# Performance work log

Hardware: AMD Instinct MI355X
Metric: run time of the kernel (lower is better)

Reference implementation:

```python
import jax, jax.numpy as jnp
import numpy as np

B, T, L = 16, 512, 128
ENC, H, E, V, A = 512, 1024, 512, 10000, 512
SOS = 1


def setup_inputs() -> dict:
    key = jax.random.key(0)
    ks = jax.random.split(key, 16)
    s = 0.02
    return {
        "enc_out": jax.random.normal(ks[0], (B, T, ENC), jnp.float32),
        "enc_lens": jax.random.randint(ks[1], (B,), T // 2, T + 1),
        "ys": jax.random.randint(ks[2], (B, L), 3, V),
        "embed": jax.random.normal(ks[3], (V, E), jnp.float32) * s,
        "W_ih0": jax.random.normal(ks[4], (4 * H, E + ENC), jnp.float32) * s,
        "W_hh0": jax.random.normal(ks[5], (4 * H, H), jnp.float32) * s,
        "b0": jnp.zeros((4 * H,), jnp.float32),
        "W_ih1": jax.random.normal(ks[6], (4 * H, H), jnp.float32) * s,
        "W_hh1": jax.random.normal(ks[7], (4 * H, H), jnp.float32) * s,
        "b1": jnp.zeros((4 * H,), jnp.float32),
        "W_enc": jax.random.normal(ks[8], (ENC, A), jnp.float32) * s,
        "b_att": jnp.zeros((A,), jnp.float32),
        "v_att": jax.random.normal(ks[9], (A,), jnp.float32) * s,
        "W_dec": jax.random.normal(ks[10], (H, A), jnp.float32) * s,
        "W_bn": jax.random.normal(ks[11], (H + ENC, H), jnp.float32) * s,
        "b_bn": jnp.zeros((H,), jnp.float32),
        "W_out": jax.random.normal(ks[12], (H, V), jnp.float32) * s,
        "b_out": jnp.zeros((V,), jnp.float32),
    }


def _lstm_cell(x, h, c, W_ih, W_hh, b):
    # torch.nn.LSTMCell gate order: i, f, g, o
    g = x @ W_ih.T + h @ W_hh.T + b
    i, f, gg, o = jnp.split(g, 4, axis=-1)
    c = jax.nn.sigmoid(f) * c + jax.nn.sigmoid(i) * jnp.tanh(gg)
    h = jax.nn.sigmoid(o) * jnp.tanh(c)
    return h, c


def reference(enc_out, enc_lens, ys, embed, W_ih0, W_hh0, b0, W_ih1, W_hh1, b1,
              W_enc, b_att, v_att, W_dec, W_bn, b_bn, W_out, b_out):
    # teacher forcing: ys_in = [<sos>, y_1..y_L]  -> [B, L+1]
    ys_in = jnp.concatenate([jnp.full((B, 1), SOS, ys.dtype), ys], axis=1)
    ys_emb = embed[ys_in]                       # [B, L+1, E]
    enc_proj = enc_out @ W_enc                  # [B, T, A], precomputed once
    mask = jnp.arange(T)[None, :] < enc_lens[:, None]  # [B, T]
    z = jnp.zeros((B, H), jnp.float32)
    carry0 = (z, z, z, z, jnp.zeros((B, ENC), jnp.float32))

    def step(carry, y_emb_t):
        h0, c0, h1, c1, ctx = carry
        x0 = jnp.concatenate([y_emb_t, ctx], axis=-1)          # emb + context feed
        h0, c0 = _lstm_cell(x0, h0, c0, W_ih0, W_hh0, b0)
        h1n, c1 = _lstm_cell(h0, h1, c1, W_ih1, W_hh1, b1)
        dec = h1n + h0                                          # residual connection
        # additive content-based attention
        e = jnp.tanh(enc_proj + (dec @ W_dec)[:, None, :] + b_att) @ v_att  # [B, T]
        aw = jax.nn.softmax(jnp.where(mask, e, -1e9), axis=-1)
        ctx = jnp.einsum('bt,btd->bd', aw, enc_out)             # [B, ENC]
        attn_v = jnp.tanh(jnp.concatenate([dec, ctx], axis=-1) @ W_bn + b_bn)
        logits = attn_v @ W_out + b_out                          # logits_temp = 1.0
        return (h0, c0, h1n, c1, ctx), logits

    _, logits = jax.lax.scan(step, carry0, jnp.swapaxes(ys_emb, 0, 1))
    return jnp.swapaxes(logits, 0, 1)           # [B, L+1, V]
```

## Files before the change

kernel.cpp:

```cpp
#include <hip/hip_runtime.h>
#include <hip/hip_bf16.h>
#include <cstddef>

#define B_ 16
#define T_ 512
#define L_ 128
#define NSTEP 129
#define ENC_ 512
#define H_ 1024
#define E_ 512
#define V_ 10000
#define A_ 512
#define SOS_ 1

typedef __hip_bfloat16 bf16;
typedef __attribute__((ext_vector_type(4))) float f32x4;
typedef __attribute__((ext_vector_type(8))) short short8;

__device__ __forceinline__ float sigm(float x) { return 1.0f / (1.0f + expf(-x)); }
__device__ __forceinline__ unsigned int f2bu(float f) {
    bf16 h = __float2bfloat16(f);
    return (unsigned int)*(unsigned short*)&h;
}
__device__ __forceinline__ float bu2f(unsigned int u) { return __uint_as_float(u << 16); }

__global__ void zero_kernel(float* __restrict__ p, int n4) {
    int i = blockIdx.x * blockDim.x + threadIdx.x;
    if (i < n4) {
        float4 z = {0.f, 0.f, 0.f, 0.f};
        *(float4*)(p + (size_t)i * 4) = z;
    }
}

__global__ __launch_bounds__(256) void cvt_bf16_kernel(const float* __restrict__ in,
                                                       bf16* __restrict__ out, int n4) {
    int i = blockIdx.x * 256 + threadIdx.x;
    if (i < n4) {
        float4 v = *(const float4*)(in + (size_t)i * 4);
        uint2 pk;
        pk.x = f2bu(v.x) | (f2bu(v.y) << 16);
        pk.y = f2bu(v.z) | (f2bu(v.w) << 16);
        *(uint2*)(out + (size_t)i * 4) = pk;
    }
}

__global__ __launch_bounds__(256) void transpose_kernel(const float* __restrict__ in,
                                                        bf16* __restrict__ out, int R, int C) {
    __shared__ float tile[32][33];
    int c0 = blockIdx.x * 32, r0 = blockIdx.y * 32;
    int tx = threadIdx.x & 31, ty = threadIdx.x >> 5;
#pragma unroll
    for (int i = 0; i < 4; ++i) {
        int r = r0 + ty + i * 8, c = c0 + tx;
        if (c < C) tile[ty + i * 8][tx] = in[(size_t)r * C + c];
    }
    __syncthreads();
#pragma unroll
    for (int i = 0; i < 4; ++i) {
        int c = c0 + ty + i * 8, r = r0 + tx;
        if (c < C) out[(size_t)c * R + r] = __float2bfloat16(tile[tx][ty + i * 8]);
    }
}

__global__ __launch_bounds__(256) void pack_lstm_kernel(const float* __restrict__ Wih,
                                                        const float* __restrict__ Whh,
                                                        const float* __restrict__ bsrc,
                                                        bf16* __restrict__ Wp,
                                                        float* __restrict__ bp) {
    int idx = blockIdx.x * 256 + threadIdx.x;
    int p = idx >> 9, k4 = idx & 511;
    int h = p >> 2, g = p & 3;
    int r = g * H_ + h;
    int k = k4 * 4;
    const float* src = (k < 1024) ? (Wih + (size_t)r * 1024 + k)
                                  : (Whh + (size_t)r * 1024 + (k - 1024));
    float4 v = *(const float4*)src;
    uint2 pk;
    pk.x = f2bu(v.x) | (f2bu(v.y) << 16);
    pk.y = f2bu(v.z) | (f2bu(v.w) << 16);
    *(uint2*)(Wp + (size_t)p * 2048 + k) = pk;
    if (k4 == 0) bp[p] = bsrc[r];
}

__global__ __launch_bounds__(256) void encproj_mfma(const bf16* __restrict__ Ab,
                                                    const bf16* __restrict__ Bt,
                                                    bf16* __restrict__ Cb) {
    int tid = threadIdx.x, w = tid >> 6, lane = tid & 63;
    int lm = lane & 15, hi = lane >> 4, lk = hi * 8;
    int mrow = blockIdx.x * 64 + w * 16 + lm;
    int nb = blockIdx.y * 128;
    f32x4 acc[8];
#pragma unroll
    for (int i = 0; i < 8; ++i) acc[i] = (f32x4){0.f, 0.f, 0.f, 0.f};
    for (int k0 = 0; k0 < 512; k0 += 32) {
        int kk = k0 + lk;
        short8 a = *(const short8*)(Ab + (size_t)mrow * 512 + kk);
#pragma unroll
        for (int ns = 0; ns < 8; ++ns) {
            int col = nb + ns * 16 + lm;
            short8 bf = *(const short8*)(Bt + (size_t)col * 512 + kk);
            acc[ns] = __builtin_amdgcn_mfma_f32_16x16x32_bf16(a, bf, acc[ns], 0, 0, 0);
        }
    }
#pragma unroll
    for (int ns = 0; ns < 8; ++ns) {
        int n = nb + ns * 16 + lm;
#pragma unroll
        for (int j = 0; j < 4; ++j) {
            int m = blockIdx.x * 64 + w * 16 + hi * 4 + j;
            Cb[(size_t)m * 512 + n] = __float2bfloat16(acc[ns][j]);
        }
    }
}

template <int MODE>
__global__ __launch_bounds__(256) void lstm_mfma(
    const bf16* __restrict__ Wp, const float* __restrict__ bp,
    const float* __restrict__ embed, const int* __restrict__ ys,
    const float* __restrict__ ctx_prev,
    const float* __restrict__ srcA,
    const float* __restrict__ srcB,
    float* __restrict__ cbuf, float* __restrict__ h_out,
    bf16* __restrict__ dec_allb, int t) {
    __shared__ unsigned short xb[16 * 2048];
    int tid = threadIdx.x;
    int w = tid >> 6, lane = tid & 63;
    int lm = lane & 15, hi = lane >> 4;

    for (int c = 0; c < 4; ++c) {
        for (int i = 0; i < 8; ++i) {
            int idx = tid + i * 256;
            int k4 = idx & 127, bb = idx >> 7;
            int k = k4 * 4;
            float4 v;
            if (MODE == 0) {
                if (c == 0) {
                    int y = (t == 0) ? SOS_ : ys[bb * L_ + (t - 1)];
                    v = *(const float4*)(embed + (size_t)y * E_ + k);
                } else if (c == 1) {
                    v = *(const float4*)(ctx_prev + bb * ENC_ + k);
                } else {
                    v = *(const float4*)(srcA + bb * H_ + (c - 2) * 512 + k);
                }
            } else {
                const float* sp = (c < 2) ? srcA : srcB;
                v = *(const float4*)(sp + bb * H_ + (c & 1) * 512 + k);
            }
            uint2 pk;
            pk.x = f2bu(v.x) | (f2bu(v.y) << 16);
            pk.y = f2bu(v.z) | (f2bu(v.w) << 16);
            int off = (bb * 2048 + c * 512 + k) ^ ((bb & 7) << 3);
            *(uint2*)(xb + off) = pk;
        }
    }
    __syncthreads();

    f32x4 acc = {0.f, 0.f, 0.f, 0.f};
    const bf16* wrow = Wp + ((size_t)(blockIdx.x * 16 + lm)) * 2048;
    int kw = w * 512 + hi * 8;
    int axr = (lm & 7) << 3;
#pragma unroll
    for (int ks = 0; ks < 16; ++ks) {
        int k = kw + ks * 32;
        short8 av = *(const short8*)(xb + ((lm * 2048 + k) ^ axr));
        short8 bv = *(const short8*)(wrow + k);
        acc = __builtin_amdgcn_mfma_f32_16x16x32_bf16(av, bv, acc, 0, 0, 0);
    }
    __syncthreads();
    float* red = (float*)xb;
    *(f32x4*)(red + (w * 64 + lane) * 4) = acc;
    __syncthreads();
    if (w == 0) {
        f32x4 s = acc;
#pragma unroll
        for (int ww = 1; ww < 4; ++ww) s += *(f32x4*)(red + (ww * 64 + lane) * 4);
        float bpv = bp[blockIdx.x * 16 + lm];
        float* g16 = red + 1024;
#pragma unroll
        for (int j = 0; j < 4; ++j) g16[lm * 16 + hi * 4 + j] = s[j] + bpv;
    }
    __syncthreads();
    if (tid < 64) {
        float* g16 = ((float*)xb) + 1024;
        int b = tid & 15, hl = tid >> 4;
        int h = blockIdx.x * 4 + hl;
        float gi = g16[(hl * 4 + 0) * 16 + b];
        float gf = g16[(hl * 4 + 1) * 16 + b];
        float gg = g16[(hl * 4 + 2) * 16 + b];
        float go = g16[(hl * 4 + 3) * 16 + b];
        float cold = cbuf[b * H_ + h];
        float cn = sigm(gf) * cold + sigm(gi) * tanhf(gg);
        float hn = sigm(go) * tanhf(cn);
        cbuf[b * H_ + h] = cn;
        h_out[b * H_ + h] = hn;
        if (MODE == 1) {
            float d = hn + srcA[b * H_ + h];
            dec_allb[((size_t)t * 16 + b) * H_ + h] = __float2bfloat16(d);
        }
    }
}

__global__ __launch_bounds__(256) void sgemv_mfma(const bf16* __restrict__ WdT,
                                                  const bf16* __restrict__ decb,
                                                  const float* __restrict__ b_att,
                                                  float* __restrict__ sbuf, int t) {
    __shared__ float red[4 * 64 * 4];
    int tid = threadIdx.x, w = tid >> 6, lane = tid & 63;
    int lm = lane & 15, hi = lane >> 4;
    f32x4 acc = {0.f, 0.f, 0.f, 0.f};
    const bf16* arow = decb + ((size_t)t * 16 + lm) * 1024;
    const bf16* brow = WdT + ((size_t)(blockIdx.x * 16 + lm)) * 1024;
    int kw = w * 256 + hi * 8;
#pragma unroll
    for (int ks = 0; ks < 8; ++ks) {
        int k = kw + ks * 32;
        short8 av = *(const short8*)(arow + k);
        short8 bv = *(const short8*)(brow + k);
        acc = __builtin_amdgcn_mfma_f32_16x16x32_bf16(av, bv, acc, 0, 0, 0);
    }
    *(f32x4*)(red + (w * 64 + lane) * 4) = acc;
    __syncthreads();
    if (w == 0) {
        f32x4 s = acc;
#pragma unroll
        for (int ww = 1; ww < 4; ++ww) s += *(f32x4*)(red + (ww * 64 + lane) * 4);
        float ba = b_att[blockIdx.x * 16 + lm];
#pragma unroll
        for (int j = 0; j < 4; ++j)
            sbuf[(hi * 4 + j) * A_ + blockIdx.x * 16 + lm] = s[j] + ba;
    }
}

__global__ __launch_bounds__(256) void att_e_kernel(const bf16* __restrict__ projb,
                                                    const float* __restrict__ sbuf,
                                                    const float* __restrict__ v_att,
                                                    float* __restrict__ ebuf,
                                                    float* __restrict__ ctx_next) {
    int tid = threadIdx.x;
    int flat = blockIdx.x * 256 + tid;
    if (flat < B_ * ENC_) ctx_next[flat] = 0.f;
    int wid = blockIdx.x * 4 + (tid >> 6);
    int lane = tid & 63;
    int b = wid >> 9, t = wid & 511;
    short8 p8 = *(const short8*)(projb + ((size_t)(b * T_ + t)) * A_ + lane * 8);
    float4 s0 = *(const float4*)(sbuf + b * A_ + lane * 8);
    float4 s1 = *(const float4*)(sbuf + b * A_ + lane * 8 + 4);
    float4 v0 = *(const float4*)(v_att + lane * 8);
    float4 v1 = *(const float4*)(v_att + lane * 8 + 4);
    float part = 0.f;
    part += v0.x * tanhf(bu2f((unsigned short)p8[0]) + s0.x);
    part += v0.y * tanhf(bu2f((unsigned short)p8[1]) + s0.y);
    part += v0.z * tanhf(bu2f((unsigned short)p8[2]) + s0.z);
    part += v0.w * tanhf(bu2f((unsigned short)p8[3]) + s0.w);
    part += v1.x * tanhf(bu2f((unsigned short)p8[4]) + s1.x);
    part += v1.y * tanhf(bu2f((unsigned short)p8[5]) + s1.y);
    part += v1.z * tanhf(bu2f((unsigned short)p8[6]) + s1.z);
    part += v1.w * tanhf(bu2f((unsigned short)p8[7]) + s1.w);
    for (int off = 32; off; off >>= 1) part += __shfl_xor(part, off);
    if (lane == 0) ebuf[b * T_ + t] = part;
}

__global__ __launch_bounds__(256) void att_ctx_kernel(const float* __restrict__ ebuf,
                                                      const int* __restrict__ enc_lens,
                                                      const bf16* __restrict__ enc_outb,
                                                      float* __restrict__ ctx_next) {
    int b = blockIdx.x >> 4, tc = blockIdx.x & 15;
    int tid = threadIdx.x;
    int len = enc_lens[b];
    __shared__ float red[256];
    __shared__ float aw[32];
    int t1 = tid, t2 = tid + 256;
    float e1 = ebuf[b * T_ + t1], e2 = ebuf[b * T_ + t2];
    float m1 = (t1 < len) ? e1 : -3.0e38f;
    float m2 = (t2 < len) ? e2 : -3.0e38f;
    red[tid] = fmaxf(m1, m2);
    __syncthreads();
    for (int s2 = 128; s2; s2 >>= 1) {
        if (tid < s2) red[tid] = fmaxf(red[tid], red[tid + s2]);
        __syncthreads();
    }
    float M = red[0];
    __syncthreads();
    float x1 = (t1 < len) ? expf(e1 - M) : 0.f;
    float x2 = (t2 < len) ? expf(e2 - M) : 0.f;
    red[tid] = x1 + x2;
    __syncthreads();
    for (int s2 = 128; s2; s2 >>= 1) {
        if (tid < s2) red[tid] += red[tid + s2];
        __syncthreads();
    }
    float S = red[0];
    __syncthreads();
    if (tid < 32) {
        int t = tc * 32 + tid;
        aw[tid] = (t < len) ? expf(ebuf[b * T_ + t] - M) / S : 0.f;
    }
    __syncthreads();
    float a0 = 0.f, a1 = 0.f;
    int e0 = tid * 2;
    for (int i = 0; i < 32; ++i) {
        float wgt = aw[i];
        unsigned int u = *(const unsigned int*)(enc_outb + ((size_t)(b * T_ + tc * 32 + i)) * ENC_ + e0);
        a0 += wgt * bu2f(u & 0xffffu);
        a1 += wgt * bu2f(u >> 16);
    }
    atomicAdd(&ctx_next[b * ENC_ + e0], a0);
    atomicAdd(&ctx_next[b * ENC_ + e0 + 1], a1);
}

__global__ __launch_bounds__(256) void f0_kernel(const float* __restrict__ ctx_all,
                                                 bf16* __restrict__ ctx_allb) {
    int idx = blockIdx.x * 256 + threadIdx.x;
    int r = idx >> 9, e = idx & 511;
    float v = ctx_all[((size_t)((r >> 4) + 1)) * (B_ * ENC_) + (r & 15) * ENC_ + e];
    ctx_allb[(size_t)r * ENC_ + e] = __float2bfloat16(v);
}

__global__ __launch_bounds__(256) void f1_kernel(const bf16* __restrict__ decb,
                                                 const bf16* __restrict__ ctxb,
                                                 const bf16* __restrict__ WbnT,
                                                 const float* __restrict__ b_bn,
                                                 bf16* __restrict__ avb) {
    int tid = threadIdx.x, w = tid >> 6, lane = tid & 63;
    int lm = lane & 15, lk = (lane >> 4) * 8;
    int mrow = blockIdx.x * 64 + w * 16 + lm;
    int nb = blockIdx.y * 128;
    f32x4 acc[8];
#pragma unroll
    for (int i = 0; i < 8; ++i) acc[i] = (f32x4){0.f, 0.f, 0.f, 0.f};
    for (int k0 = 0; k0 < 1536; k0 += 32) {
        int kk = k0 + lk;
        short8 a;
        if (kk < 1024)
            a = *(const short8*)(decb + (size_t)mrow * 1024 + kk);
        else
            a = *(const short8*)(ctxb + (size_t)mrow * 512 + (kk - 1024));
#pragma unroll
        for (int ns = 0; ns < 8; ++ns) {
            int col = nb + ns * 16 + lm;
            short8 bf = *(const short8*)(WbnT + (size_t)col * 1536 + kk);
            acc[ns] = __builtin_amdgcn_mfma_f32_16x16x32_bf16(a, bf, acc[ns], 0, 0, 0);
        }
    }
#pragma unroll
    for (int ns = 0; ns < 8; ++ns) {
        int n = nb + ns * 16 + lm;
#pragma unroll
        for (int j = 0; j < 4; ++j) {
            int m = blockIdx.x * 64 + w * 16 + (lane >> 4) * 4 + j;
            if (m < NSTEP * B_) {
                float v = tanhf(acc[ns][j] + b_bn[n]);
                avb[(size_t)m * 1024 + n] = __float2bfloat16(v);
            }
        }
    }
}

__global__ __launch_bounds__(256) void f2_kernel(const bf16* __restrict__ avb,
                                                 const bf16* __restrict__ WoutT,
                                                 const float* __restrict__ b_out,
                                                 float* __restrict__ out) {
    int tid = threadIdx.x, w = tid >> 6, lane = tid & 63;
    int lm = lane & 15, lk = (lane >> 4) * 8;
    int mrow = blockIdx.x * 64 + w * 16 + lm;
    int nb = blockIdx.y * 128;
    f32x4 acc[8];
#pragma unroll
    for (int i = 0; i < 8; ++i) acc[i] = (f32x4){0.f, 0.f, 0.f, 0.f};
    for (int k0 = 0; k0 < 1024; k0 += 32) {
        int kk = k0 + lk;
        short8 a = *(const short8*)(avb + (size_t)mrow * 1024 + kk);
#pragma unroll
        for (int ns = 0; ns < 8; ++ns) {
            int col = nb + ns * 16 + lm;
            short8 bf = *(const short8*)(WoutT + (size_t)col * 1024 + kk);
            acc[ns] = __builtin_amdgcn_mfma_f32_16x16x32_bf16(a, bf, acc[ns], 0, 0, 0);
        }
    }
#pragma unroll
    for (int ns = 0; ns < 8; ++ns) {
        int n = nb + ns * 16 + lm;
#pragma unroll
        for (int j = 0; j < 4; ++j) {
            int m = blockIdx.x * 64 + w * 16 + (lane >> 4) * 4 + j;
            if (m < NSTEP * B_ && n < V_) {
                int tt = m >> 4, bb = m & 15;
                out[((size_t)bb * NSTEP + tt) * V_ + n] = acc[ns][j] + b_out[n];
            }
        }
    }
}

extern "C" void kernel_launch(void* const* d_in, const int* in_sizes, int n_in, void* d_out,
                              int out_size, void* d_ws, size_t ws_size, hipStream_t stream) {
    const float* enc_out = (const float*)d_in[0];
    const int* enc_lens = (const int*)d_in[1];
    const int* ys = (const int*)d_in[2];
    const float* embed = (const float*)d_in[3];
    const float* W_ih0 = (const float*)d_in[4];
    const float* W_hh0 = (const float*)d_in[5];
    const float* b0 = (const float*)d_in[6];
    const float* W_ih1 = (const float*)d_in[7];
    const float* W_hh1 = (const float*)d_in[8];
    const float* b1 = (const float*)d_in[9];
    const float* W_enc = (const float*)d_in[10];
    const float* b_att = (const float*)d_in[11];
    const float* v_att = (const float*)d_in[12];
    const float* W_dec = (const float*)d_in[13];
    const float* W_bn = (const float*)d_in[14];
    const float* b_bn = (const float*)d_in[15];
    const float* W_out = (const float*)d_in[16];
    const float* b_out = (const float*)d_in[17];
    float* out = (float*)d_out;

    if (ws_size < (size_t)92 * 1000 * 1000) return;

    float* ws = (float*)d_ws;
    size_t o = 0;
    float* h0R0 = ws + o;    o += B_ * H_;
    float* h1R0 = ws + o;    o += B_ * H_;
    float* c0R = ws + o;     o += B_ * H_;
    float* c1R = ws + o;     o += B_ * H_;
    float* ctx_all = ws + o; o += (size_t)(NSTEP + 1) * B_ * ENC_;
    float* h0R1 = ws + o;    o += B_ * H_;
    float* h1R1 = ws + o;    o += B_ * H_;
    float* sbuf = ws + o;    o += B_ * A_;
    float* ebuf = ws + o;    o += B_ * T_;
    float* bp0 = ws + o;     o += 4 * H_;
    float* bp1 = ws + o;     o += 4 * H_;

    bf16* bb = (bf16*)(ws + o);
    size_t ob = 0;
    bf16* enc_outb = bb + ob;  ob += (size_t)B_ * T_ * ENC_;
    bf16* enc_projb = bb + ob; ob += (size_t)B_ * T_ * A_;
    bf16* Wp0 = bb + ob;       ob += (size_t)4096 * 2048;
    bf16* Wp1 = bb + ob;       ob += (size_t)4096 * 2048;
    bf16* WencT = bb + ob;     ob += (size_t)A_ * ENC_;
    bf16* WdecT = bb + ob;     ob += (size_t)A_ * H_;
    bf16* dec_allb = bb + ob;  ob += (size_t)2112 * 1024;
    bf16* ctx_allb = bb + ob;  ob += (size_t)2112 * 512;
    bf16* avb = bb + ob;       ob += (size_t)2112 * 1024;
    bf16* WbnT = bb + ob;      ob += (size_t)1024 * 1536;
    bf16* WoutT = bb + ob;     ob += (size_t)10240 * 1024;

    float* h0buf[2] = {h0R0, h0R1};
    float* h1buf[2] = {h1R0, h1R1};

    zero_kernel<<<72, 256, 0, stream>>>(h0R0, (4 * B_ * H_ + B_ * ENC_) / 4);
    cvt_bf16_kernel<<<4096, 256, 0, stream>>>(enc_out, enc_outb, B_ * T_ * ENC_ / 4);
    transpose_kernel<<<dim3(16, 16), 256, 0, stream>>>(W_enc, WencT, ENC_, A_);
    transpose_kernel<<<dim3(16, 32), 256, 0, stream>>>(W_dec, WdecT, H_, A_);
    transpose_kernel<<<dim3(32, 48), 256, 0, stream>>>(W_bn, WbnT, H_ + ENC_, H_);
    transpose_kernel<<<dim3(313, 32), 256, 0, stream>>>(W_out, WoutT, H_, V_);
    pack_lstm_kernel<<<8192, 256, 0, stream>>>(W_ih0, W_hh0, b0, Wp0, bp0);
    pack_lstm_kernel<<<8192, 256, 0, stream>>>(W_ih1, W_hh1, b1, Wp1, bp1);
    encproj_mfma<<<dim3(128, 4), 256, 0, stream>>>(enc_outb, WencT, enc_projb);

    for (int t = 0; t < NSTEP; ++t) {
        int cur = t & 1;
        lstm_mfma<0><<<256, 256, 0, stream>>>(Wp0, bp0, embed, ys,
                                              ctx_all + (size_t)t * B_ * ENC_, h0buf[cur],
                                              nullptr, c0R, h0buf[cur ^ 1], nullptr, t);
        lstm_mfma<1><<<256, 256, 0, stream>>>(Wp1, bp1, nullptr, nullptr, nullptr,
                                              h0buf[cur ^ 1], h1buf[cur], c1R, h1buf[cur ^ 1],
                                              dec_allb, t);
        sgemv_mfma<<<32, 256, 0, stream>>>(WdecT, dec_allb, b_att, sbuf, t);
        att_e_kernel<<<2048, 256, 0, stream>>>(enc_projb, sbuf, v_att, ebuf,
                                               ctx_all + (size_t)(t + 1) * B_ * ENC_);
        att_ctx_kernel<<<256, 256, 0, stream>>>(ebuf, enc_lens, enc_outb,
                                                ctx_all + (size_t)(t + 1) * B_ * ENC_);
    }

    f0_kernel<<<(NSTEP * B_ * ENC_) / 256, 256, 0, stream>>>(ctx_all, ctx_allb);
    f1_kernel<<<dim3(33, 8), 256, 0, stream>>>(dec_allb, ctx_allb, WbnT, b_bn, avb);
    f2_kernel<<<dim3(33, 79), 256, 0, stream>>>(avb, WoutT, b_out, out);
}
```

Before: 4.856 ms.

## Fuse attention score and context kernels using deferred softmax normalization

Merges the per-step attention energy kernel and the softmax/context kernel into one kernel. Each block computes exp of its 32 energies without a max shift, atomically accumulates the unnormalized context numerator and the denominator, and skips chunks past the sequence length. The division by the denominator moves into the consumers: the next LSTM step's input load and the final context conversion. This removes one launch, the global energy buffer round trip and the block-wide max/sum reductions per step. In exchange, exp without max subtraction could overflow for large energies, and the results depend on the order of atomic float additions.

```diff
diff --git a/kernel.cpp b/kernel.cpp
--- a/kernel.cpp
+++ b/kernel.cpp
@@ -30,6 +30,10 @@
         float4 z = {0.f, 0.f, 0.f, 0.f};
         *(float4*)(p + (size_t)i * 4) = z;
     }
+}
+
+__global__ void den1_kernel(float* __restrict__ d) {
+    if (threadIdx.x < 16) d[threadIdx.x] = 1.0f;
 }
 
 __global__ __launch_bounds__(256) void cvt_bf16_kernel(const float* __restrict__ in,
@@ -117,7 +121,7 @@
 __global__ __launch_bounds__(256) void lstm_mfma(
     const bf16* __restrict__ Wp, const float* __restrict__ bp,
     const float* __restrict__ embed, const int* __restrict__ ys,
-    const float* __restrict__ ctx_prev,
+    const float* __restrict__ num_prev, const float* __restrict__ den_prev,
     const float* __restrict__ srcA,
     const float* __restrict__ srcB,
     float* __restrict__ cbuf, float* __restrict__ h_out,
@@ -138,7 +142,10 @@
                     int y = (t == 0) ? SOS_ : ys[bb * L_ + (t - 1)];
                     v = *(const float4*)(embed + (size_t)y * E_ + k);
                 } else if (c == 1) {
-                    v = *(const float4*)(ctx_prev + bb * ENC_ + k);
+                    float4 nv = *(const float4*)(num_prev + bb * ENC_ + k);
+                    float dinv = 1.0f / den_prev[bb];
+                    v.x = nv.x * dinv; v.y = nv.y * dinv;
+                    v.z = nv.z * dinv; v.w = nv.w * dinv;
                 } else {
                     v = *(const float4*)(srcA + bb * H_ + (c - 2) * 512 + k);
                 }
@@ -231,88 +238,70 @@
     }
 }
 
-__global__ __launch_bounds__(256) void att_e_kernel(const bf16* __restrict__ projb,
-                                                    const float* __restrict__ sbuf,
-                                                    const float* __restrict__ v_att,
-                                                    float* __restrict__ ebuf,
-                                                    float* __restrict__ ctx_next) {
-    int tid = threadIdx.x;
-    int flat = blockIdx.x * 256 + tid;
-    if (flat < B_ * ENC_) ctx_next[flat] = 0.f;
-    int wid = blockIdx.x * 4 + (tid >> 6);
-    int lane = tid & 63;
-    int b = wid >> 9, t = wid & 511;
-    short8 p8 = *(const short8*)(projb + ((size_t)(b * T_ + t)) * A_ + lane * 8);
+__global__ __launch_bounds__(256) void att_fused_kernel(const bf16* __restrict__ projb,
+                                                        const float* __restrict__ sbuf,
+                                                        const float* __restrict__ v_att,
+                                                        const int* __restrict__ enc_lens,
+                                                        const bf16* __restrict__ enc_outb,
+                                                        float* __restrict__ num_next,
+                                                        float* __restrict__ den_next) {
+    int bid = blockIdx.x;
+    int b = bid >> 4, tc = bid & 15;
+    int t0 = tc * 32;
+    int len = enc_lens[b];
+    if (t0 >= len) return;
+    int tid = threadIdx.x, w = tid >> 6, lane = tid & 63;
+    __shared__ float ew[32];
+
     float4 s0 = *(const float4*)(sbuf + b * A_ + lane * 8);
     float4 s1 = *(const float4*)(sbuf + b * A_ + lane * 8 + 4);
     float4 v0 = *(const float4*)(v_att + lane * 8);
     float4 v1 = *(const float4*)(v_att + lane * 8 + 4);
-    float part = 0.f;
-    part += v0.x * tanhf(bu2f((unsigned short)p8[0]) + s0.x);
-    part += v0.y * tanhf(bu2f((unsigned short)p8[1]) + s0.y);
-    part += v0.z * tanhf(bu2f((unsigned short)p8[2]) + s0.z);
-    part += v0.w * tanhf(bu2f((unsigned short)p8[3]) + s0.w);
-    part += v1.x * tanhf(bu2f((unsigned short)p8[4]) + s1.x);
-    part += v1.y * tanhf(bu2f((unsigned short)p8[5]) + s1.y);
-    part += v1.z * tanhf(bu2f((unsigned short)p8[6]) + s1.z);
-    part += v1.w * tanhf(bu2f((unsigned short)p8[7]) + s1.w);
-    for (int off = 32; off; off >>= 1) part += __shfl_xor(part, off);
-    if (lane == 0) ebuf[b * T_ + t] = part;
-}
-
-__global__ __launch_bounds__(256) void att_ctx_kernel(const float* __restrict__ ebuf,
-                                                      const int* __restrict__ enc_lens,
-                                                      const bf16* __restrict__ enc_outb,
-                                                      float* __restrict__ ctx_next) {
-    int b = blockIdx.x >> 4, tc = blockIdx.x & 15;
-    int tid = threadIdx.x;
-    int len = enc_lens[b];
-    __shared__ float red[256];
-    __shared__ float aw[32];
-    int t1 = tid, t2 = tid + 256;
-    float e1 = ebuf[b * T_ + t1], e2 = ebuf[b * T_ + t2];
-    float m1 = (t1 < len) ? e1 : -3.0e38f;
-    float m2 = (t2 < len) ? e2 : -3.0e38f;
-    red[tid] = fmaxf(m1, m2);
-    __syncthreads();
-    for (int s2 = 128; s2; s2 >>= 1) {
-        if (tid < s2) red[tid] = fmaxf(red[tid], red[tid + s2]);
-        __syncthreads();
-    }
-    float M = red[0];
-    __syncthreads();
-    float x1 = (t1 < len) ? expf(e1 - M) : 0.f;
-    float x2 = (t2 < len) ? expf(e2 - M) : 0.f;
-    red[tid] = x1 + x2;
-    __syncthreads();
-    for (int s2 = 128; s2; s2 >>= 1) {
-        if (tid < s2) red[tid] += red[tid + s2];
-        __syncthreads();
-    }
-    float S = red[0];
-    __syncthreads();
-    if (tid < 32) {
-        int t = tc * 32 + tid;
-        aw[tid] = (t < len) ? expf(ebuf[b * T_ + t] - M) / S : 0.f;
-    }
-    __syncthreads();
+
+#pragma unroll
+    for (int i = 0; i < 8; ++i) {
+        int t = t0 + w * 8 + i;
+        short8 p8 = *(const short8*)(projb + ((size_t)(b * T_ + t)) * A_ + lane * 8);
+        float part = 0.f;
+        part += v0.x * tanhf(bu2f((unsigned short)p8[0]) + s0.x);
+        part += v0.y * tanhf(bu2f((unsigned short)p8[1]) + s0.y);
+        part += v0.z * tanhf(bu2f((unsigned short)p8[2]) + s0.z);
+        part += v0.w * tanhf(bu2f((unsigned short)p8[3]) + s0.w);
+        part += v1.x * tanhf(bu2f((unsigned short)p8[4]) + s1.x);
+        part += v1.y * tanhf(bu2f((unsigned short)p8[5]) + s1.y);
+        part += v1.z * tanhf(bu2f((unsigned short)p8[6]) + s1.z);
+        part += v1.w * tanhf(bu2f((unsigned short)p8[7]) + s1.w);
+        for (int off = 32; off; off >>= 1) part += __shfl_xor(part, off);
+        if (lane == 0) ew[w * 8 + i] = (t < len) ? expf(part) : 0.f;
+    }
+    __syncthreads();
+    if (tid == 0) {
+        float sden = 0.f;
+#pragma unroll
+        for (int i = 0; i < 32; ++i) sden += ew[i];
+        atomicAdd(den_next + b, sden);
+    }
     float a0 = 0.f, a1 = 0.f;
     int e0 = tid * 2;
     for (int i = 0; i < 32; ++i) {
-        float wgt = aw[i];
-        unsigned int u = *(const unsigned int*)(enc_outb + ((size_t)(b * T_ + tc * 32 + i)) * ENC_ + e0);
+        float wgt = ew[i];
+        unsigned int u =
+            *(const unsigned int*)(enc_outb + ((size_t)(b * T_ + t0 + i)) * ENC_ + e0);
         a0 += wgt * bu2f(u & 0xffffu);
         a1 += wgt * bu2f(u >> 16);
     }
-    atomicAdd(&ctx_next[b * ENC_ + e0], a0);
-    atomicAdd(&ctx_next[b * ENC_ + e0 + 1], a1);
-}
-
-__global__ __launch_bounds__(256) void f0_kernel(const float* __restrict__ ctx_all,
+    atomicAdd(num_next + b * ENC_ + e0, a0);
+    atomicAdd(num_next + b * ENC_ + e0 + 1, a1);
+}
+
+__global__ __launch_bounds__(256) void f0_kernel(const float* __restrict__ num_all,
+                                                 const float* __restrict__ den_all,
                                                  bf16* __restrict__ ctx_allb) {
     int idx = blockIdx.x * 256 + threadIdx.x;
     int r = idx >> 9, e = idx & 511;
-    float v = ctx_all[((size_t)((r >> 4) + 1)) * (B_ * ENC_) + (r & 15) * ENC_ + e];
+    int t = r >> 4, b = r & 15;
+    float v = num_all[((size_t)(t + 1)) * (B_ * ENC_) + b * ENC_ + e] /
+              den_all[(t + 1) * B_ + b];
     ctx_allb[(size_t)r * ENC_ + e] = __float2bfloat16(v);
 }
 
@@ -421,11 +410,12 @@
     float* h1R0 = ws + o;    o += B_ * H_;
     float* c0R = ws + o;     o += B_ * H_;
     float* c1R = ws + o;     o += B_ * H_;
-    float* ctx_all = ws + o; o += (size_t)(NSTEP + 1) * B_ * ENC_;
+    float* num_all = ws + o; o += (size_t)(NSTEP + 1) * B_ * ENC_;
+    float* den_all = ws + o; o += (size_t)(NSTEP + 1) * B_;
+    size_t zero_f32 = o;
     float* h0R1 = ws + o;    o += B_ * H_;
     float* h1R1 = ws + o;    o += B_ * H_;
     float* sbuf = ws + o;    o += B_ * A_;
-    float* ebuf = ws + o;    o += B_ * T_;
     float* bp0 = ws + o;     o += 4 * H_;
     float* bp1 = ws + o;     o += 4 * H_;
 
@@ -446,7 +436,11 @@
     float* h0buf[2] = {h0R0, h0R1};
     float* h1buf[2] = {h1R0, h1R1};
 
-    zero_kernel<<<72, 256, 0, stream>>>(h0R0, (4 * B_ * H_ + B_ * ENC_) / 4);
+    {
+        int n4 = (int)((zero_f32 + 3) / 4);
+        zero_kernel<<<(n4 + 255) / 256, 256, 0, stream>>>(ws, n4);
+    }
+    den1_kernel<<<1, 64, 0, stream>>>(den_all);
     cvt_bf16_kernel<<<4096, 256, 0, stream>>>(enc_out, enc_outb, B_ * T_ * ENC_ / 4);
     transpose_kernel<<<dim3(16, 16), 256, 0, stream>>>(W_enc, WencT, ENC_, A_);
     transpose_kernel<<<dim3(16, 32), 256, 0, stream>>>(W_dec, WdecT, H_, A_);
@@ -459,19 +453,19 @@
     for (int t = 0; t < NSTEP; ++t) {
         int cur = t & 1;
         lstm_mfma<0><<<256, 256, 0, stream>>>(Wp0, bp0, embed, ys,
-                                              ctx_all + (size_t)t * B_ * ENC_, h0buf[cur],
-                                              nullptr, c0R, h0buf[cur ^ 1], nullptr, t);
-        lstm_mfma<1><<<256, 256, 0, stream>>>(Wp1, bp1, nullptr, nullptr, nullptr,
+                                              num_all + (size_t)t * B_ * ENC_,
+                                              den_all + (size_t)t * B_, h0buf[cur], nullptr,
+                                              c0R, h0buf[cur ^ 1], nullptr, t);
+        lstm_mfma<1><<<256, 256, 0, stream>>>(Wp1, bp1, nullptr, nullptr, nullptr, nullptr,
                                               h0buf[cur ^ 1], h1buf[cur], c1R, h1buf[cur ^ 1],
                                               dec_allb, t);
         sgemv_mfma<<<32, 256, 0, stream>>>(WdecT, dec_allb, b_att, sbuf, t);
-        att_e_kernel<<<2048, 256, 0, stream>>>(enc_projb, sbuf, v_att, ebuf,
-                                               ctx_all + (size_t)(t + 1) * B_ * ENC_);
-        att_ctx_kernel<<<256, 256, 0, stream>>>(ebuf, enc_lens, enc_outb,
-                                                ctx_all + (size_t)(t + 1) * B_ * ENC_);
-    }
-
-    f0_kernel<<<(NSTEP * B_ * ENC_) / 256, 256, 0, stream>>>(ctx_all, ctx_allb);
+        att_fused_kernel<<<256, 256, 0, stream>>>(enc_projb, sbuf, v_att, enc_lens, enc_outb,
+                                                  num_all + (size_t)(t + 1) * B_ * ENC_,
+                                                  den_all + (size_t)(t + 1) * B_);
+    }
+
+    f0_kernel<<<(NSTEP * B_ * ENC_) / 256, 256, 0, stream>>>(num_all, den_all, ctx_allb);
     f1_kernel<<<dim3(33, 8), 256, 0, stream>>>(dec_allb, ctx_allb, WbnT, b_bn, avb);
     f2_kernel<<<dim3(33, 79), 256, 0, stream>>>(avb, WoutT, b_out, out);
 }
```

New measurement: 5.555 ms. 1.14x slower.
